# Kernel tuning notes

Hardware: AMD Instinct MI355X
Metric: run time of the kernel (lower is better)

The kernel has to match this reference:

```python
import jax, jax.numpy as jnp
import numpy as np

TOP_K = 8
N_EXPERTS = 256
N_GROUP = 8
TOPK_GROUP = 4
SCALE = 2.5


def setup_inputs() -> dict:
    key = jax.random.key(0)
    k1, k2, k3 = jax.random.split(key, 3)
    hidden_states = jax.random.normal(k1, (4, 2048, 7168), dtype=jnp.float32)
    weight = jax.random.normal(k2, (N_EXPERTS, 7168), dtype=jnp.float32) * 0.02
    e_score_correction_bias = jax.random.normal(k3, (N_EXPERTS,), dtype=jnp.float32) * 0.1
    return {"hidden_states": hidden_states, "weight": weight,
            "e_score_correction_bias": e_score_correction_bias}


def reference(hidden_states, weight, e_score_correction_bias):
    B, S, H = hidden_states.shape
    x = hidden_states.reshape(-1, H).astype(jnp.float32)          # [T, H]
    router_logits = jnp.einsum('th,eh->te', x, weight)            # [T, E]
    scores = jax.nn.sigmoid(router_logits)                        # [T, E]
    scores_b = scores + e_score_correction_bias[None, :]          # bias-corrected
    T = x.shape[0]
    # per-group score = sum of top-2 bias-corrected scores in the group
    grouped = scores_b.reshape(T, N_GROUP, N_EXPERTS // N_GROUP)
    group_scores = jax.lax.top_k(grouped, 2)[0].sum(-1)           # [T, G]
    group_idx = jax.lax.top_k(group_scores, TOPK_GROUP)[1]        # [T, topk_group]
    group_mask = jax.nn.one_hot(group_idx, N_GROUP, dtype=jnp.bool_).any(axis=1)  # [T, G]
    expert_mask = jnp.repeat(group_mask, N_EXPERTS // N_GROUP, axis=-1)           # [T, E]
    masked = jnp.where(expert_mask, scores_b, -jnp.inf)
    _, topk_indices = jax.lax.top_k(masked, TOP_K)                # [T, top_k]
    topk_weights = jnp.take_along_axis(scores, topk_indices, axis=-1)  # un-biased scores
    topk_weights = topk_weights / jnp.sum(topk_weights, axis=-1, keepdims=True)
    topk_weights = topk_weights * SCALE
    return topk_indices, topk_weights
```

## Files before the change

kernel.cpp:

```cpp
#include <hip/hip_runtime.h>
#include <math.h>

typedef __attribute__((ext_vector_type(4))) float f32x4;
typedef _Float16 f16;
typedef __attribute__((ext_vector_type(8))) _Float16 f16x8;

constexpr int H       = 7168;
constexpr int E       = 256;
constexpr int T_TOTAL = 8192;

constexpr int KSPLIT  = 4;
constexpr int K_SLICE = H / KSPLIT;
constexpr int NCH     = K_SLICE / 64;
constexpr int NPAIR   = NCH / 2;
constexpr int MT      = 64;

constexpr int N_GROUP    = 8;
constexpr int TOPK_GROUP = 4;
constexpr int TOP_K      = 8;

constexpr size_t SCORES_OFF = 8u * 1024 * 1024;

__global__ __launch_bounds__(64) void pack_w_kernel(const float* __restrict__ w,
                                                    f16* __restrict__ wf)
{
    const int l  = threadIdx.x;
    const int nt = blockIdx.x & 15;
    const int kc = blockIdx.x >> 4;
    const int e  = nt * 16 + (l & 15);
    const int h  = kc * 32 + (l >> 4) * 8;
    const float* src = &w[(size_t)e * H + h];
    f32x4 v0 = *reinterpret_cast<const f32x4*>(src);
    f32x4 v1 = *reinterpret_cast<const f32x4*>(src + 4);
    float v[8] = {v0[0], v0[1], v0[2], v0[3], v1[0], v1[1], v1[2], v1[3]};
    f16x8 hi, lo;
    #pragma unroll
    for (int j = 0; j < 8; ++j) {
        f16 h16 = (f16)v[j];
        hi[j] = h16;
        lo[j] = (f16)(v[j] - (float)h16);
    }
    const size_t base = (((size_t)kc * 16 + nt) * 2) * 512 + (size_t)l * 8;
    *reinterpret_cast<f16x8*>(&wf[base])       = hi;
    *reinterpret_cast<f16x8*>(&wf[base + 512]) = lo;
}

__global__ __launch_bounds__(512, 4) void gemm_kernel(
    const float* __restrict__ x,
    const f16*   __restrict__ wf,
    float* __restrict__ scores)
{
    __shared__ __align__(16) f16 x_lds[2][2][4 * 2 * 2 * 512];

    const int tid  = threadIdx.x;
    const int lane = tid & 63;
    const int wn   = tid >> 6;

    const int bid = blockIdx.x;
    const int ksl = bid & 3;
    const int mb  = bid >> 2;
    const int t0  = mb * MT;
    const int k0  = ksl * K_SLICE;
    const int kc0 = k0 >> 5;

    const int lmt = (tid >> 6) & 3;
    const int lks = tid >> 8;
    const float* xrow = &x[(size_t)(t0 + lmt * 16 + (lane & 15)) * H
                           + k0 + lks * 32 + (lane >> 4) * 8];

    const int lm = lane & 15;
    const int kq = lane >> 4;

    f32x4 acc[4][2];
    #pragma unroll
    for (int mt = 0; mt < 4; ++mt)
        #pragma unroll
        for (int nt = 0; nt < 2; ++nt)
            acc[mt][nt] = (f32x4){0.f, 0.f, 0.f, 0.f};

    auto stage = [&](int bu, int half, f32x4 v0, f32x4 v1) {
        float v[8] = {v0[0], v0[1], v0[2], v0[3], v1[0], v1[1], v1[2], v1[3]};
        f16x8 hi, lo;
        #pragma unroll
        for (int j = 0; j < 8; ++j) {
            f16 h16 = (f16)v[j];
            hi[j] = h16;
            lo[j] = (f16)(v[j] - (float)h16);
        }
        f16* base = &x_lds[bu][half][((lmt * 2 + lks) * 2) * 512 + lane * 8];
        *reinterpret_cast<f16x8*>(base)       = hi;
        *reinterpret_cast<f16x8*>(base + 512) = lo;
    };

    auto load_b = [&](f16x8 (&b)[2][2], int kc) {
        #pragma unroll
        for (int nt = 0; nt < 2; ++nt)
            #pragma unroll
            for (int s = 0; s < 2; ++s)
                b[nt][s] = *reinterpret_cast<const f16x8*>(
                    &wf[(((size_t)kc * 16 + wn * 2 + nt) * 2 + s) * 512 + lane * 8]);
    };

    auto mfma_step = [&](const f16x8 (&b)[2][2], int bu, int half, int ks) {
        #pragma unroll
        for (int mt = 0; mt < 4; ++mt) {
            const f16* ap = &x_lds[bu][half][((mt * 2 + ks) * 2) * 512 + lane * 8];
            f16x8 ahi = *reinterpret_cast<const f16x8*>(ap);
            f16x8 alo = *reinterpret_cast<const f16x8*>(ap + 512);
            acc[mt][0] = __builtin_amdgcn_mfma_f32_16x16x32_f16(ahi, b[0][0], acc[mt][0], 0, 0, 0);
            acc[mt][1] = __builtin_amdgcn_mfma_f32_16x16x32_f16(ahi, b[1][0], acc[mt][1], 0, 0, 0);
            acc[mt][0] = __builtin_amdgcn_mfma_f32_16x16x32_f16(ahi, b[0][1], acc[mt][0], 0, 0, 0);
            acc[mt][1] = __builtin_amdgcn_mfma_f32_16x16x32_f16(ahi, b[1][1], acc[mt][1], 0, 0, 0);
            acc[mt][0] = __builtin_amdgcn_mfma_f32_16x16x32_f16(alo, b[0][0], acc[mt][0], 0, 0, 0);
            acc[mt][1] = __builtin_amdgcn_mfma_f32_16x16x32_f16(alo, b[1][0], acc[mt][1], 0, 0, 0);
        }
    };

    f16x8 b0[2][2], b1[2][2];

    {
        f32x4 v0 = *reinterpret_cast<const f32x4*>(xrow);
        f32x4 v1 = *reinterpret_cast<const f32x4*>(xrow + 4);
        f32x4 v2 = *reinterpret_cast<const f32x4*>(xrow + 64);
        f32x4 v3 = *reinterpret_cast<const f32x4*>(xrow + 68);
        stage(0, 0, v0, v1);
        stage(0, 1, v2, v3);
    }
    load_b(b0, kc0);
    __syncthreads();

    for (int i = 0; i < NPAIR; ++i) {
        const int buf   = i & 1;
        const int kbase = kc0 + i * 4;
        const bool last = (i + 1 == NPAIR);

        f32x4 nva0, nva1, nvb0, nvb1;
        if (!last) {
            const float* nx = xrow + (2 * i + 2) * 64;
            nva0 = *reinterpret_cast<const f32x4*>(nx);
            nva1 = *reinterpret_cast<const f32x4*>(nx + 4);
            nvb0 = *reinterpret_cast<const f32x4*>(nx + 64);
            nvb1 = *reinterpret_cast<const f32x4*>(nx + 68);
        }

        load_b(b1, kbase + 1);
        __builtin_amdgcn_s_setprio(1);
        mfma_step(b0, buf, 0, 0);
        load_b(b0, kbase + 2);
        mfma_step(b1, buf, 0, 1);
        load_b(b1, kbase + 3);
        mfma_step(b0, buf, 1, 0);
        load_b(b0, last ? kc0 : (kbase + 4));
        mfma_step(b1, buf, 1, 1);
        __builtin_amdgcn_s_setprio(0);

        if (!last) {
            stage(buf ^ 1, 0, nva0, nva1);
            stage(buf ^ 1, 1, nvb0, nvb1);
            asm volatile("s_waitcnt lgkmcnt(0)" ::: "memory");
            __builtin_amdgcn_s_barrier();
            asm volatile("" ::: "memory");
        }
    }

    #pragma unroll
    for (int mt = 0; mt < 4; ++mt)
        #pragma unroll
        for (int nt = 0; nt < 2; ++nt)
            #pragma unroll
            for (int r = 0; r < 4; ++r) {
                const int tok = mt * 16 + kq * 4 + r;
                const int e   = wn * 32 + nt * 16 + lm;
                scores[(((size_t)(t0 + tok)) * KSPLIT + ksl) * E + e] = acc[mt][nt][r];
            }
}

__global__ __launch_bounds__(256) void gate_kernel(
    const float* __restrict__ scores,
    const float* __restrict__ bias,
    float* __restrict__ out)
{
    const int lane = threadIdx.x & 63;
    const int wv   = threadIdx.x >> 6;
    const int t    = blockIdx.x * 4 + wv;

    const float* p = &scores[(size_t)t * (KSPLIT * E) + lane * 4];
    f32x4 s = (f32x4){0.f, 0.f, 0.f, 0.f};
    #pragma unroll
    for (int k = 0; k < KSPLIT; ++k)
        s += *reinterpret_cast<const f32x4*>(p + k * E);
    f32x4 bi = *reinterpret_cast<const f32x4*>(&bias[lane * 4]);

    float sig[4], bsc[4];
    #pragma unroll
    for (int j = 0; j < 4; ++j) {
        sig[j] = 1.0f / (1.0f + expf(-s[j]));
        bsc[j] = sig[j] + bi[j];
    }

    float h01 = fmaxf(bsc[0], bsc[1]), l01 = fminf(bsc[0], bsc[1]);
    float h23 = fmaxf(bsc[2], bsc[3]), l23 = fminf(bsc[2], bsc[3]);
    float m1 = fmaxf(h01, h23);
    float m2 = fmaxf(fminf(h01, h23), fmaxf(l01, l23));
    #pragma unroll
    for (int d = 1; d < 8; d <<= 1) {
        float om1 = __shfl_xor(m1, d);
        float om2 = __shfl_xor(m2, d);
        float nm1 = fmaxf(m1, om1);
        float nm2 = fmaxf(fminf(m1, om1), fmaxf(m2, om2));
        m1 = nm1; m2 = nm2;
    }
    const float gs  = m1 + m2;
    const int   gid = lane >> 3;

    int cnt = 0;
    #pragma unroll
    for (int j = 0; j < N_GROUP; ++j) {
        float gsj = __shfl(gs, j * 8);
        cnt += (gsj > gs || (gsj == gs && j < gid)) ? 1 : 0;
    }
    const bool sel = (cnt < TOPK_GROUP);

    float mb[4];
    #pragma unroll
    for (int j = 0; j < 4; ++j) mb[j] = sel ? bsc[j] : -INFINITY;

    float wsum = 0.f;
    f32x4 iv0, iv1, wv0, wv1;
    #pragma unroll
    for (int r = 0; r < TOP_K; ++r) {
        float v = mb[0]; int li = 0;
        if (mb[1] > v) { v = mb[1]; li = 1; }
        if (mb[2] > v) { v = mb[2]; li = 2; }
        if (mb[3] > v) { v = mb[3]; li = 3; }
        int ei = lane * 4 + li;
        #pragma unroll
        for (int d = 1; d < 64; d <<= 1) {
            float ov = __shfl_xor(v, d);
            int   oi = __shfl_xor(ei, d);
            if (ov > v || (ov == v && oi < ei)) { v = ov; ei = oi; }
        }
        const int sub = ei & 3, owner = ei >> 2;
        const float svl = (sub & 2) ? ((sub & 1) ? sig[3] : sig[2])
                                    : ((sub & 1) ? sig[1] : sig[0]);
        const float wr = __shfl(svl, owner);
        #pragma unroll
        for (int j = 0; j < 4; ++j)
            if (lane == owner && j == sub) mb[j] = -INFINITY;
        wsum += wr;
        if (r < 4) { iv0[r] = (float)ei;     wv0[r] = wr; }
        else       { iv1[r - 4] = (float)ei; wv1[r - 4] = wr; }
    }

    const float scale = 2.5f / wsum;
    #pragma unroll
    for (int j = 0; j < 4; ++j) { wv0[j] *= scale; wv1[j] *= scale; }

    if (lane == 0) {
        float* oi_ = out + (size_t)t * TOP_K;
        float* ow_ = out + (size_t)T_TOTAL * TOP_K + (size_t)t * TOP_K;
        *reinterpret_cast<f32x4*>(oi_)     = iv0;
        *reinterpret_cast<f32x4*>(oi_ + 4) = iv1;
        *reinterpret_cast<f32x4*>(ow_)     = wv0;
        *reinterpret_cast<f32x4*>(ow_ + 4) = wv1;
    }
}

extern "C" void kernel_launch(void* const* d_in, const int* in_sizes, int n_in,
                              void* d_out, int out_size, void* d_ws, size_t ws_size,
                              hipStream_t stream) {
    const float* x    = (const float*)d_in[0];
    const float* w    = (const float*)d_in[1];
    const float* bias = (const float*)d_in[2];
    float* out = (float*)d_out;

    f16*   wf     = (f16*)d_ws;
    float* scores = (float*)((char*)d_ws + SCORES_OFF);

    hipLaunchKernelGGL(pack_w_kernel, dim3((H / 32) * 16), dim3(64), 0, stream, w, wf);
    hipLaunchKernelGGL(gemm_kernel, dim3((T_TOTAL / MT) * KSPLIT), dim3(512), 0, stream,
                       x, wf, scores);
    hipLaunchKernelGGL(gate_kernel, dim3(T_TOTAL / 4), dim3(256), 0, stream,
                       scores, bias, out);
}
```

Baseline: 372.1 us.

## Fuse gating into GEMM via last-arriving split-K block with atomic counter

New measurement: 638.5 us. +71.6%, slower.

```diff
diff --git a/kernel.cpp b/kernel.cpp
--- a/kernel.cpp
+++ b/kernel.cpp
@@ -14,17 +14,24 @@
 constexpr int NCH     = K_SLICE / 64;
 constexpr int NPAIR   = NCH / 2;
 constexpr int MT      = 64;
+constexpr int NMB     = T_TOTAL / MT;
 
 constexpr int N_GROUP    = 8;
 constexpr int TOPK_GROUP = 4;
 constexpr int TOP_K      = 8;
 
 constexpr size_t SCORES_OFF = 8u * 1024 * 1024;
+constexpr size_t CNT_OFF    = 48u * 1024 * 1024;
 
 __global__ __launch_bounds__(64) void pack_w_kernel(const float* __restrict__ w,
-                                                    f16* __restrict__ wf)
+                                                    f16* __restrict__ wf,
+                                                    unsigned* __restrict__ cnt)
 {
     const int l  = threadIdx.x;
+    if (blockIdx.x == 0) {
+        #pragma unroll
+        for (int i = 0; i < NMB / 64; ++i) cnt[i * 64 + l] = 0u;
+    }
     const int nt = blockIdx.x & 15;
     const int kc = blockIdx.x >> 4;
     const int e  = nt * 16 + (l & 15);
@@ -48,9 +55,13 @@
 __global__ __launch_bounds__(512, 4) void gemm_kernel(
     const float* __restrict__ x,
     const f16*   __restrict__ wf,
-    float* __restrict__ scores)
+    float* __restrict__ scores,
+    const float* __restrict__ bias,
+    float* __restrict__ out,
+    unsigned* __restrict__ cnt)
 {
     __shared__ __align__(16) f16 x_lds[2][2][4 * 2 * 2 * 512];
+    __shared__ int sh_last;
 
     const int tid  = threadIdx.x;
     const int lane = tid & 63;
@@ -173,96 +184,98 @@
                 const int e   = wn * 32 + nt * 16 + lm;
                 scores[(((size_t)(t0 + tok)) * KSPLIT + ksl) * E + e] = acc[mt][nt][r];
             }
-}
-
-__global__ __launch_bounds__(256) void gate_kernel(
-    const float* __restrict__ scores,
-    const float* __restrict__ bias,
-    float* __restrict__ out)
-{
-    const int lane = threadIdx.x & 63;
-    const int wv   = threadIdx.x >> 6;
-    const int t    = blockIdx.x * 4 + wv;
-
-    const float* p = &scores[(size_t)t * (KSPLIT * E) + lane * 4];
-    f32x4 s = (f32x4){0.f, 0.f, 0.f, 0.f};
-    #pragma unroll
-    for (int k = 0; k < KSPLIT; ++k)
-        s += *reinterpret_cast<const f32x4*>(p + k * E);
-    f32x4 bi = *reinterpret_cast<const f32x4*>(&bias[lane * 4]);
-
-    float sig[4], bsc[4];
-    #pragma unroll
-    for (int j = 0; j < 4; ++j) {
-        sig[j] = 1.0f / (1.0f + expf(-s[j]));
-        bsc[j] = sig[j] + bi[j];
-    }
-
-    float h01 = fmaxf(bsc[0], bsc[1]), l01 = fminf(bsc[0], bsc[1]);
-    float h23 = fmaxf(bsc[2], bsc[3]), l23 = fminf(bsc[2], bsc[3]);
-    float m1 = fmaxf(h01, h23);
-    float m2 = fmaxf(fminf(h01, h23), fmaxf(l01, l23));
-    #pragma unroll
-    for (int d = 1; d < 8; d <<= 1) {
-        float om1 = __shfl_xor(m1, d);
-        float om2 = __shfl_xor(m2, d);
-        float nm1 = fmaxf(m1, om1);
-        float nm2 = fmaxf(fminf(m1, om1), fmaxf(m2, om2));
-        m1 = nm1; m2 = nm2;
-    }
-    const float gs  = m1 + m2;
-    const int   gid = lane >> 3;
-
-    int cnt = 0;
-    #pragma unroll
-    for (int j = 0; j < N_GROUP; ++j) {
-        float gsj = __shfl(gs, j * 8);
-        cnt += (gsj > gs || (gsj == gs && j < gid)) ? 1 : 0;
-    }
-    const bool sel = (cnt < TOPK_GROUP);
-
-    float mb[4];
-    #pragma unroll
-    for (int j = 0; j < 4; ++j) mb[j] = sel ? bsc[j] : -INFINITY;
-
-    float wsum = 0.f;
-    f32x4 iv0, iv1, wv0, wv1;
-    #pragma unroll
-    for (int r = 0; r < TOP_K; ++r) {
-        float v = mb[0]; int li = 0;
-        if (mb[1] > v) { v = mb[1]; li = 1; }
-        if (mb[2] > v) { v = mb[2]; li = 2; }
-        if (mb[3] > v) { v = mb[3]; li = 3; }
-        int ei = lane * 4 + li;
-        #pragma unroll
-        for (int d = 1; d < 64; d <<= 1) {
-            float ov = __shfl_xor(v, d);
-            int   oi = __shfl_xor(ei, d);
-            if (ov > v || (ov == v && oi < ei)) { v = ov; ei = oi; }
-        }
-        const int sub = ei & 3, owner = ei >> 2;
-        const float svl = (sub & 2) ? ((sub & 1) ? sig[3] : sig[2])
-                                    : ((sub & 1) ? sig[1] : sig[0]);
-        const float wr = __shfl(svl, owner);
-        #pragma unroll
-        for (int j = 0; j < 4; ++j)
-            if (lane == owner && j == sub) mb[j] = -INFINITY;
-        wsum += wr;
-        if (r < 4) { iv0[r] = (float)ei;     wv0[r] = wr; }
-        else       { iv1[r - 4] = (float)ei; wv1[r - 4] = wr; }
-    }
-
-    const float scale = 2.5f / wsum;
-    #pragma unroll
-    for (int j = 0; j < 4; ++j) { wv0[j] *= scale; wv1[j] *= scale; }
-
-    if (lane == 0) {
-        float* oi_ = out + (size_t)t * TOP_K;
-        float* ow_ = out + (size_t)T_TOTAL * TOP_K + (size_t)t * TOP_K;
-        *reinterpret_cast<f32x4*>(oi_)     = iv0;
-        *reinterpret_cast<f32x4*>(oi_ + 4) = iv1;
-        *reinterpret_cast<f32x4*>(ow_)     = wv0;
-        *reinterpret_cast<f32x4*>(ow_ + 4) = wv1;
+
+    __threadfence();
+    __syncthreads();
+    if (tid == 0)
+        sh_last = (atomicAdd(&cnt[mb], 1u) == KSPLIT - 1) ? 1 : 0;
+    __syncthreads();
+    if (!sh_last) return;
+    __threadfence();
+
+    for (int rep = 0; rep < MT / 8; ++rep) {
+        const int t = t0 + rep * 8 + wn;
+
+        const float* p = &scores[(size_t)t * (KSPLIT * E) + lane * 4];
+        f32x4 s = (f32x4){0.f, 0.f, 0.f, 0.f};
+        #pragma unroll
+        for (int k = 0; k < KSPLIT; ++k)
+            s += *reinterpret_cast<const f32x4*>(p + k * E);
+        f32x4 bi = *reinterpret_cast<const f32x4*>(&bias[lane * 4]);
+
+        float sig[4], bsc[4];
+        #pragma unroll
+        for (int j = 0; j < 4; ++j) {
+            sig[j] = 1.0f / (1.0f + expf(-s[j]));
+            bsc[j] = sig[j] + bi[j];
+        }
+
+        float h01 = fmaxf(bsc[0], bsc[1]), l01 = fminf(bsc[0], bsc[1]);
+        float h23 = fmaxf(bsc[2], bsc[3]), l23 = fminf(bsc[2], bsc[3]);
+        float m1 = fmaxf(h01, h23);
+        float m2 = fmaxf(fminf(h01, h23), fmaxf(l01, l23));
+        #pragma unroll
+        for (int d = 1; d < 8; d <<= 1) {
+            float om1 = __shfl_xor(m1, d);
+            float om2 = __shfl_xor(m2, d);
+            float nm1 = fmaxf(m1, om1);
+            float nm2 = fmaxf(fminf(m1, om1), fmaxf(m2, om2));
+            m1 = nm1; m2 = nm2;
+        }
+        const float gs  = m1 + m2;
+        const int   gid = lane >> 3;
+
+        int cntg = 0;
+        #pragma unroll
+        for (int j = 0; j < N_GROUP; ++j) {
+            float gsj = __shfl(gs, j * 8);
+            cntg += (gsj > gs || (gsj == gs && j < gid)) ? 1 : 0;
+        }
+        const bool selg = (cntg < TOPK_GROUP);
+
+        float mbv[4];
+        #pragma unroll
+        for (int j = 0; j < 4; ++j) mbv[j] = selg ? bsc[j] : -INFINITY;
+
+        float wsum = 0.f;
+        f32x4 iv0, iv1, wv0, wv1;
+        #pragma unroll
+        for (int r = 0; r < TOP_K; ++r) {
+            float v = mbv[0]; int li = 0;
+            if (mbv[1] > v) { v = mbv[1]; li = 1; }
+            if (mbv[2] > v) { v = mbv[2]; li = 2; }
+            if (mbv[3] > v) { v = mbv[3]; li = 3; }
+            int ei = lane * 4 + li;
+            #pragma unroll
+            for (int d = 1; d < 64; d <<= 1) {
+                float ov = __shfl_xor(v, d);
+                int   oi = __shfl_xor(ei, d);
+                if (ov > v || (ov == v && oi < ei)) { v = ov; ei = oi; }
+            }
+            const int sub = ei & 3, owner = ei >> 2;
+            const float svl = (sub & 2) ? ((sub & 1) ? sig[3] : sig[2])
+                                        : ((sub & 1) ? sig[1] : sig[0]);
+            const float wr = __shfl(svl, owner);
+            #pragma unroll
+            for (int j = 0; j < 4; ++j)
+                if (lane == owner && j == sub) mbv[j] = -INFINITY;
+            wsum += wr;
+            if (r < 4) { iv0[r] = (float)ei;     wv0[r] = wr; }
+            else       { iv1[r - 4] = (float)ei; wv1[r - 4] = wr; }
+        }
+
+        const float scale = 2.5f / wsum;
+        #pragma unroll
+        for (int j = 0; j < 4; ++j) { wv0[j] *= scale; wv1[j] *= scale; }
+
+        if (lane == 0) {
+            float* oi_ = out + (size_t)t * TOP_K;
+            float* ow_ = out + (size_t)T_TOTAL * TOP_K + (size_t)t * TOP_K;
+            *reinterpret_cast<f32x4*>(oi_)     = iv0;
+            *reinterpret_cast<f32x4*>(oi_ + 4) = iv1;
+            *reinterpret_cast<f32x4*>(ow_)     = wv0;
+            *reinterpret_cast<f32x4*>(ow_ + 4) = wv1;
+        }
     }
 }
 
@@ -274,12 +287,12 @@
     const float* bias = (const float*)d_in[2];
     float* out = (float*)d_out;
 
-    f16*   wf     = (f16*)d_ws;
-    float* scores = (float*)((char*)d_ws + SCORES_OFF);
-
-    hipLaunchKernelGGL(pack_w_kernel, dim3((H / 32) * 16), dim3(64), 0, stream, w, wf);
+    f16*      wf     = (f16*)d_ws;
+    float*    scores = (float*)((char*)d_ws + SCORES_OFF);
+    unsigned* cnt    = (unsigned*)((char*)d_ws + CNT_OFF);
+
+    hipLaunchKernelGGL(pack_w_kernel, dim3((H / 32) * 16), dim3(64), 0, stream,
+                       w, wf, cnt);
     hipLaunchKernelGGL(gemm_kernel, dim3((T_TOTAL / MT) * KSPLIT), dim3(512), 0, stream,
-                       x, wf, scores);
-    hipLaunchKernelGGL(gate_kernel, dim3(T_TOTAL / 4), dim3(256), 0, stream,
-                       scores, bias, out);
+                       x, wf, scores, bias, out, cnt);
 }
```
